# Kernel tuning notes

Hardware: AMD Instinct MI355X
Metric: run time of the kernel (lower is better)

The kernel has to match this reference:

```python
import jax, jax.numpy as jnp
import numpy as np

# constants matching init_kwargs
CLASSES = 80
CONF_T = 0.05
IOU_T = 0.5
MAX_DET = 100
MAX_DET_PER_CLASS = 100


def setup_inputs() -> dict:
    key = jax.random.key(0)
    k1, k2, k3, k4 = jax.random.split(key, 4)
    B, N = 8, 2048
    # structured predictions: [x1, y1, x2, y2, class, score] in a 640x640 image
    xy1 = jax.random.uniform(k1, (B, N, 2), dtype=jnp.float32) * 580.0
    wh = jax.random.uniform(k2, (B, N, 2), dtype=jnp.float32) * 60.0 + 1.0
    cls = jax.random.randint(k3, (B, N), 0, CLASSES).astype(jnp.float32)
    sc = jax.random.uniform(k4, (B, N), dtype=jnp.float32)
    predictions = jnp.concatenate([xy1, xy1 + wh, cls[..., None], sc[..., None]], axis=-1)
    return {"predictions": predictions}


def _pairwise_iou(b):
    # b: [B, N, 4] xyxy (IoU is invariant under xyxy<->yxyx swap used by the layer)
    x1, y1, x2, y2 = b[..., 0], b[..., 1], b[..., 2], b[..., 3]
    area = jnp.maximum(x2 - x1, 0.0) * jnp.maximum(y2 - y1, 0.0)  # [B,N]
    ix1 = jnp.maximum(x1[:, :, None], x1[:, None, :])
    iy1 = jnp.maximum(y1[:, :, None], y1[:, None, :])
    ix2 = jnp.minimum(x2[:, :, None], x2[:, None, :])
    iy2 = jnp.minimum(y2[:, :, None], y2[:, None, :])
    inter = jnp.maximum(ix2 - ix1, 0.0) * jnp.maximum(iy2 - iy1, 0.0)  # [B,N,N]
    union = area[:, :, None] + area[:, None, :] - inter
    return inter / jnp.maximum(union, 1e-8)


def reference(predictions):
    # Combined per-class NMS. Because scores are one-hot over classes (score *
    # one_hot(class)), per-class NMS is equivalent to class-aware greedy NMS on
    # the globally score-sorted boxes where suppression only acts within a class.
    B, N, _ = predictions.shape
    boxes = predictions[..., :4]
    cls = predictions[..., 4].astype(jnp.int32)
    scores = predictions[..., 5]
    valid = scores > CONF_T

    # sort by score descending (invalid boxes pushed to the end)
    order = jnp.argsort(jnp.where(valid, scores, -jnp.inf), axis=1)[:, ::-1]  # [B,N]
    bsort = jnp.take_along_axis(boxes, order[..., None], axis=1)
    ssort = jnp.take_along_axis(scores, order, axis=1)
    csort = jnp.take_along_axis(cls, order, axis=1)
    vsort = jnp.take_along_axis(valid, order, axis=1)

    iou = _pairwise_iou(bsort)  # [B,N,N]
    same_cls = csort[:, :, None] == csort[:, None, :]
    sup_mat = same_cls & (iou > IOU_T)  # [B,N,N] bool

    idxs = jnp.arange(N)

    def body(i, keep):
        active = keep[:, i]  # [B] is box i still alive?
        sup = keep & sup_mat[:, i, :] & (idxs > i)[None, :]
        return jnp.where(active[:, None], keep & ~sup, keep)

    keep = jax.lax.fori_loop(0, N, body, vsort)  # [B,N]

    # per-class cap (max_detections_per_class): rank among kept boxes of same class
    oh = jax.nn.one_hot(csort, CLASSES, dtype=jnp.float32)  # [B,N,C]
    csum = jnp.cumsum(oh * keep[..., None].astype(jnp.float32), axis=1)
    rank = jnp.take_along_axis(csum, csort[..., None], axis=2)[..., 0]  # [B,N]
    keep = keep & (rank <= MAX_DET_PER_CLASS)

    # global top max_detections among kept boxes
    final = jnp.where(keep, ssort, -1.0)
    _, ti = jax.lax.top_k(final, MAX_DET)  # [B,MAX_DET]
    v = jnp.take_along_axis(keep, ti, axis=1)
    boxes_out = jnp.where(v[..., None], jnp.take_along_axis(bsort, ti[..., None], axis=1), 0.0)
    scores_out = jnp.where(v, jnp.take_along_axis(ssort, ti, axis=1), 0.0)
    classes_out = jnp.where(v, jnp.take_along_axis(csort, ti, axis=1).astype(jnp.float32), 0.0)
    num_det = jnp.sum(v, axis=1).astype(jnp.int32)
    return boxes_out, scores_out, classes_out, num_det
```

## Files before the change

kernel.cpp:

```cpp
#include <hip/hip_runtime.h>
#include <stdint.h>

#define NB 2048
#define NCLASSES 80
#define CONF_T 0.05f
#define IOU_T 0.5f
#define MAX_DET 100
#define MAX_PER_CLASS 100

typedef unsigned long long u64;
typedef unsigned int u32;
typedef unsigned char u8;

__device__ __forceinline__ u64 shfl_xor_u64(u64 v, int mask) {
    int lo = (int)(u32)v, hi = (int)(u32)(v >> 32);
    lo = __shfl_xor(lo, mask, 64);
    hi = __shfl_xor(hi, mask, 64);
    return ((u64)(u32)hi << 32) | (u32)lo;
}

__device__ __forceinline__ int sbucket(u32 bits) {
    int b = (int)(bits >> 17) - 0x1E80;
    return b < 0 ? 0 : (b > 511 ? 511 : b);
}

__global__ __launch_bounds__(512) void k_class(const float* __restrict__ pred,
                                               u8* __restrict__ supBytes) {
    const int idx = blockIdx.x, tid = threadIdx.x;
    const int lane = tid & 63, wave = tid >> 6;

    __shared__ __align__(16) char smem[49152];
    float2* csS  = (float2*)smem;
    u64*    wkey = (u64*)(smem + 16384);
    float4* wb4  = (float4*)(smem + 20480);
    u64*    wm   = (u64*)(smem + 28672);
    u8*     fst  = (u8*)(smem + 32768);

    const int b = idx / 10;
    const int c = (idx % 10) * 8 + wave;
    const float* P = pred + (size_t)b * NB * 6;
    u8* sb = supBytes + (size_t)b * NB;

    for (int i = tid; i < NB; i += 512)
        csS[i] = *reinterpret_cast<const float2*>(P + i * 6 + 4);
    __syncthreads();

    u64* wkeyW = wkey + wave * 64;
    float4* wb4W = wb4 + wave * 64;
    u64* wmW = wm + wave * 64;

    int cnt = 0;
    for (int base = 0; base < NB; base += 64) {
        int i = base + lane;
        float2 cs = csS[i];
        bool v = (cs.y > CONF_T) && ((int)cs.x == c);
        u64 m = __ballot(v);
        if (v) {
            int pos = cnt + __popcll(m & ((1ull << lane) - 1ull));
            if (pos < 64) {
                float2 p01 = *reinterpret_cast<const float2*>(P + i * 6);
                float2 p23 = *reinterpret_cast<const float2*>(P + i * 6 + 2);
                wkeyW[pos] = ((u64)__float_as_uint(cs.y) << 32) | (u32)i;
                wb4W[pos] = make_float4(p01.x, p01.y, p23.x, p23.y);
            }
        }
        cnt += __popcll(m);
    }
    __builtin_amdgcn_wave_barrier();

    if (cnt <= 64) {
        u64 mykey = 0ull; int orig = 0;
        float x1 = 0.f, y1 = 0.f, x2 = 0.f, y2 = 0.f, ar = 0.f;
        if (lane < cnt) {
            mykey = wkeyW[lane];
            orig = (int)(u32)mykey;
            float4 bx = wb4W[lane];
            x1 = bx.x; y1 = bx.y; x2 = bx.z; y2 = bx.w;
            ar = fmaxf(x2 - x1, 0.f) * fmaxf(y2 - y1, 0.f);
        }
        u64 mj = 0ull;
        if (lane < cnt) {
            for (int i = 0; i < cnt; ++i) {
                u64 ki = wkeyW[i];
                if (ki > mykey) {
                    float4 bi = wb4W[i];
                    float ari = fmaxf(bi.z - bi.x, 0.f) * fmaxf(bi.w - bi.y, 0.f);
                    float ix1 = fmaxf(bi.x, x1), iy1 = fmaxf(bi.y, y1);
                    float ix2 = fminf(bi.z, x2), iy2 = fminf(bi.w, y2);
                    float inter = fmaxf(ix2 - ix1, 0.f) * fmaxf(iy2 - iy1, 0.f);
                    float uni = ari + ar - inter;
                    if (inter / fmaxf(uni, 1e-8f) > IOU_T) mj |= 1ull << i;
                }
            }
        }
        u64 conf = __ballot(mj != 0ull);
        bool sup = false;
        if (conf != 0ull) {
            u64 srcs = mj;
            #pragma unroll
            for (int d = 1; d < 64; d <<= 1) srcs |= shfl_xor_u64(srcs, d);
            wmW[lane] = mj;
            __builtin_amdgcn_wave_barrier();
            u64 Cset = srcs | conf;
            u64 keptS2 = 0ull, rem = Cset;
            while (rem) {
                u64 t = rem, bestk = 0ull; int bi = -1;
                while (t) {
                    int i = __ffsll(t) - 1; t &= t - 1;
                    u64 k = wkeyW[i];
                    if (k > bestk) { bestk = k; bi = i; }
                }
                rem &= ~(1ull << bi);
                if ((wmW[bi] & keptS2) == 0ull) keptS2 |= 1ull << bi;
            }
            sup = (mj & keptS2) != 0ull;
        }
        if (lane < cnt) sb[orig] = sup ? 1 : 0;
    } else {
        volatile u8* vf = fst + wave * NB;
        for (int o = lane; o < NB; o += 64) vf[o] = 0;
        __builtin_amdgcn_wave_barrier();
        int keptCount = 0;
        for (;;) {
            u64 best = 0ull; int bo = -1;
            for (int o = lane; o < NB; o += 64) {
                if (vf[o]) continue;
                float2 cs = csS[o];
                if (cs.y > CONF_T && (int)cs.x == c) {
                    u64 k = ((u64)__float_as_uint(cs.y) << 32) | (u32)o;
                    if (k > best) { best = k; bo = o; }
                }
            }
            for (int d = 32; d >= 1; d >>= 1) {
                u64 ob = shfl_xor_u64(best, d);
                int obo = __shfl_xor(bo, d, 64);
                if (ob > best) { best = ob; bo = obo; }
            }
            if (best == 0ull) break;
            keptCount++;
            int orig = (int)(u32)best;
            if (lane == 0) {
                vf[orig] = 1;
                sb[orig] = (keptCount > MAX_PER_CLASS) ? 1 : 0;
            }
            __builtin_amdgcn_wave_barrier();
            const float* q = P + orig * 6;
            float ax1 = q[0], ay1 = q[1], ax2 = q[2], ay2 = q[3];
            float aar = fmaxf(ax2 - ax1, 0.f) * fmaxf(ay2 - ay1, 0.f);
            for (int o = lane; o < NB; o += 64) {
                if (vf[o]) continue;
                float2 cs = csS[o];
                if (cs.y > CONF_T && (int)cs.x == c) {
                    const float* q2 = P + o * 6;
                    float bx1 = q2[0], by1 = q2[1], bx2 = q2[2], by2 = q2[3];
                    float br = fmaxf(bx2 - bx1, 0.f) * fmaxf(by2 - by1, 0.f);
                    float ix1 = fmaxf(ax1, bx1), iy1 = fmaxf(ay1, by1);
                    float ix2 = fminf(ax2, bx2), iy2 = fminf(ay2, by2);
                    float inter = fmaxf(ix2 - ix1, 0.f) * fmaxf(iy2 - iy1, 0.f);
                    if (inter / fmaxf(aar + br - inter, 1e-8f) > IOU_T) {
                        vf[o] = 2;
                        sb[o] = 1;
                    }
                }
            }
            __builtin_amdgcn_wave_barrier();
        }
    }
}

__global__ __launch_bounds__(256) void k_sel(const float* __restrict__ pred,
                                             const u8* __restrict__ supBytes,
                                             float* __restrict__ out, int B) {
    const int b = blockIdx.x, tid = threadIdx.x;
    __shared__ u32 smw[NB / 4];
    __shared__ int hist[512];
    __shared__ u64 cand[256];
    __shared__ u64 skey[NB];
    __shared__ int candCnt, TS, keptT;

    const float* P = pred + (size_t)b * NB * 6;
    const u32* sw = (const u32*)(supBytes + (size_t)b * NB);
    for (int i = tid; i < NB / 4; i += 256) smw[i] = sw[i];
    for (int i = tid; i < 512; i += 256) hist[i] = 0;
    if (tid == 0) candCnt = 0;
    __syncthreads();

    u64 kreg[8];
    #pragma unroll
    for (int t = 0; t < 8; ++t) {
        int i = tid + t * 256;
        float s = P[i * 6 + 5];
        bool sup = ((smw[i >> 2] >> ((i & 3) * 8)) & 0xFFu) != 0u;
        u64 kk = 0ull;
        if (s > CONF_T && !sup) {
            u32 bits = __float_as_uint(s);
            kk = ((u64)bits << 32) | (u32)i;
            atomicAdd(&hist[sbucket(bits)], 1);
        }
        kreg[t] = kk;
    }
    __syncthreads();

    if (tid < 64) {
        int h[8], s = 0;
        #pragma unroll
        for (int t = 0; t < 8; ++t) { h[t] = hist[tid * 8 + t]; s += h[t]; }
        int v = s;
        #pragma unroll
        for (int d = 1; d < 64; d <<= 1) {
            int t2 = __shfl_down(v, d, 64);
            if (tid + d < 64) v += t2;
        }
        int total = __shfl(v, 0, 64);
        int target = total < MAX_DET ? total : MAX_DET;
        int run = v - s, bestB = -1;
        for (int t = 7; t >= 0; --t) {
            run += h[t];
            if (run >= target && bestB < 0) bestB = tid * 8 + t;
        }
        int T = bestB;
        #pragma unroll
        for (int d = 32; d >= 1; d >>= 1) {
            int o = __shfl_xor(T, d, 64);
            T = o > T ? o : T;
        }
        if (tid == 0) { TS = T; keptT = total; }
    }
    __syncthreads();

    const int T = TS;
    #pragma unroll
    for (int t = 0; t < 8; ++t) {
        u64 kk = kreg[t];
        if (kk != 0ull && sbucket((u32)(kk >> 32)) >= T) {
            int pos = atomicAdd(&candCnt, 1);
            if (pos < 256) cand[pos] = kk;
        }
    }
    __syncthreads();

    int cc = candCnt;
    if (cc <= 256) {
        if (tid < 64) {
            const int lane = tid;
            const int iA = lane, iB = 64 + lane, iC = 128 + lane, iD = 192 + lane;
            u64 A  = (iA < cc) ? cand[iA] : 0ull;
            u64 Bv = (iB < cc) ? cand[iB] : 0ull;
            u64 C  = (iC < cc) ? cand[iC] : 0ull;
            u64 D  = (iD < cc) ? cand[iD] : 0ull;

            auto loc = [&](u64& X, u64& Y, int ix, int k) {
                bool up = ((ix & k) == 0);
                u64 mx = X > Y ? X : Y, mn = X > Y ? Y : X;
                X = up ? mx : mn; Y = up ? mn : mx;
            };
            auto shf = [&](u64& V, int iv, int j, int k) {
                u64 p = shfl_xor_u64(V, j);
                bool low = ((lane & j) == 0);
                bool up  = ((iv & k) == 0);
                V = (low == up) ? (V > p ? V : p) : (V < p ? V : p);
            };
            for (int k = 2; k <= 256; k <<= 1) {
                int jstart = k >> 1;
                if (jstart >= 128) { loc(A, C, iA, k); loc(Bv, D, iB, k); }
                if (jstart >= 64)  { loc(A, Bv, iA, k); loc(C, D, iC, k); }
                for (int j = (jstart > 32 ? 32 : jstart); j >= 1; j >>= 1) {
                    shf(A, iA, j, k); shf(Bv, iB, j, k); shf(C, iC, j, k); shf(D, iD, j, k);
                }
            }
            skey[iA] = A; skey[iB] = Bv; skey[iC] = C; skey[iD] = D;
        }
    } else {
        #pragma unroll
        for (int t = 0; t < 8; ++t) skey[tid + t * 256] = kreg[t];
        __syncthreads();
        for (int k = 2; k <= NB; k <<= 1)
            for (int j = k >> 1; j > 0; j >>= 1) {
                for (int pp = tid; pp < (NB >> 1); pp += 256) {
                    int i1 = ((pp & ~(j - 1)) << 1) | (pp & (j - 1));
                    int i2 = i1 + j;
                    bool up = ((i1 & k) == 0);
                    u64 a = skey[i1], c2 = skey[i2];
                    if (up ? (a < c2) : (a > c2)) { skey[i1] = c2; skey[i2] = a; }
                }
                __syncthreads();
            }
    }
    __syncthreads();

    float* boxes_out   = out + (size_t)b * MAX_DET * 4;
    float* scores_out  = out + (size_t)B * MAX_DET * 4 + (size_t)b * MAX_DET;
    float* classes_out = out + (size_t)B * MAX_DET * 5 + (size_t)b * MAX_DET;
    float* numdet_out  = out + (size_t)B * MAX_DET * 6 + b;

    int nd = keptT < MAX_DET ? keptT : MAX_DET;
    if (tid < MAX_DET) {
        if (tid < nd) {
            u64 kk = skey[tid];
            int orig = (int)(u32)kk;
            const float* q = P + orig * 6;
            boxes_out[tid * 4 + 0] = q[0];
            boxes_out[tid * 4 + 1] = q[1];
            boxes_out[tid * 4 + 2] = q[2];
            boxes_out[tid * 4 + 3] = q[3];
            scores_out[tid]  = __uint_as_float((u32)(kk >> 32));
            classes_out[tid] = q[4];
        } else {
            boxes_out[tid * 4 + 0] = 0.f;
            boxes_out[tid * 4 + 1] = 0.f;
            boxes_out[tid * 4 + 2] = 0.f;
            boxes_out[tid * 4 + 3] = 0.f;
            scores_out[tid]  = 0.f;
            classes_out[tid] = 0.f;
        }
    }
    if (tid == 0) *numdet_out = (float)nd;
}

__global__ __launch_bounds__(1024) void nms_fallback(const float* __restrict__ pred,
                                                     float* __restrict__ out, int B) {
    const int b = blockIdx.x, tid = threadIdx.x;
    __shared__ u64 keys[NB];
    __shared__ float bx1[NB], by1[NB], bx2[NB], by2[NB];
    __shared__ int kc[NB];
    __shared__ int cnt[NCLASSES];
    __shared__ int overflow;
    const float* P = pred + (size_t)b * NB * 6;
    for (int i = tid; i < NB; i += 1024) {
        float s = P[i * 6 + 5];
        keys[i] = (s > CONF_T) ? (((u64)__float_as_uint(s) << 32) | (uint32_t)i)
                               : (u64)(uint32_t)i;
    }
    __syncthreads();
    for (int k = 2; k <= NB; k <<= 1)
        for (int j = k >> 1; j > 0; j >>= 1) {
            for (int i = tid; i < NB; i += 1024) {
                int ixj = i ^ j;
                if (ixj > i) {
                    u64 a = keys[i], c = keys[ixj];
                    bool up = ((i & k) == 0);
                    if (up ? (a < c) : (a > c)) { keys[i] = c; keys[ixj] = a; }
                }
            }
            __syncthreads();
        }
    for (int i = tid; i < NB; i += 1024) {
        u64 k = keys[i];
        int orig = (int)(uint32_t)k;
        const float* q = P + orig * 6;
        bx1[i] = q[0]; by1[i] = q[1]; bx2[i] = q[2]; by2[i] = q[3];
        kc[i] = ((k >> 32) != 0) ? (int)q[4] : -1;
    }
    __syncthreads();
    bool dirty = false;
    for (int i = 0; i < NB - 1; ++i) {
        if (i == 0 || dirty) { __syncthreads(); dirty = false; }
        int ci = kc[i];
        if (ci < 0) continue;
        dirty = true;
        float x1i = bx1[i], y1i = by1[i], x2i = bx2[i], y2i = by2[i];
        float ai = fmaxf(x2i - x1i, 0.f) * fmaxf(y2i - y1i, 0.f);
        for (int j = i + 1 + tid; j < NB; j += 1024) {
            if (kc[j] != ci) continue;
            float ix1 = fmaxf(x1i, bx1[j]), iy1 = fmaxf(y1i, by1[j]);
            float ix2 = fminf(x2i, bx2[j]), iy2 = fminf(y2i, by2[j]);
            float inter = fmaxf(ix2 - ix1, 0.f) * fmaxf(iy2 - iy1, 0.f);
            float aj = fmaxf(bx2[j] - bx1[j], 0.f) * fmaxf(by2[j] - by1[j], 0.f);
            if (inter / fmaxf(ai + aj - inter, 1e-8f) > IOU_T) kc[j] = -1;
        }
    }
    __syncthreads();
    for (int i = tid; i < NCLASSES; i += 1024) cnt[i] = 0;
    if (tid == 0) overflow = 0;
    __syncthreads();
    for (int i = tid; i < NB; i += 1024) if (kc[i] >= 0) atomicAdd(&cnt[kc[i]], 1);
    __syncthreads();
    if (tid < NCLASSES && cnt[tid] > MAX_PER_CLASS) atomicOr(&overflow, 1);
    __syncthreads();
    if (overflow) {
        if (tid == 0) {
            for (int c = 0; c < NCLASSES; ++c) cnt[c] = 0;
            for (int i = 0; i < NB; ++i)
                if (kc[i] >= 0 && ++cnt[kc[i]] > MAX_PER_CLASS) kc[i] = -1;
        }
        __syncthreads();
    }
    if (tid < 64) {
        const int lane = tid;
        float* boxes_out   = out + (size_t)b * MAX_DET * 4;
        float* scores_out  = out + (size_t)B * MAX_DET * 4 + (size_t)b * MAX_DET;
        float* classes_out = out + (size_t)B * MAX_DET * 5 + (size_t)b * MAX_DET;
        float* numdet_out  = out + (size_t)B * MAX_DET * 6 + b;
        int running = 0;
        for (int chunk = 0; chunk < NB / 64; ++chunk) {
            int j = chunk * 64 + lane;
            int c = kc[j];
            bool k = (c >= 0);
            u64 m = __ballot(k);
            int pos = running + __popcll(m & ((1ull << lane) - 1ull));
            if (k && pos < MAX_DET) {
                boxes_out[pos * 4 + 0] = bx1[j];
                boxes_out[pos * 4 + 1] = by1[j];
                boxes_out[pos * 4 + 2] = bx2[j];
                boxes_out[pos * 4 + 3] = by2[j];
                scores_out[pos]  = __uint_as_float((uint32_t)(keys[j] >> 32));
                classes_out[pos] = (float)c;
            }
            running += __popcll(m);
        }
        int nd = running < MAX_DET ? running : MAX_DET;
        for (int p = nd + lane; p < MAX_DET; p += 64) {
            boxes_out[p * 4 + 0] = 0.f; boxes_out[p * 4 + 1] = 0.f;
            boxes_out[p * 4 + 2] = 0.f; boxes_out[p * 4 + 3] = 0.f;
            scores_out[p] = 0.f; classes_out[p] = 0.f;
        }
        if (lane == 0) *numdet_out = (float)nd;
    }
}

extern "C" void kernel_launch(void* const* d_in, const int* in_sizes, int n_in,
                              void* d_out, int out_size, void* d_ws, size_t ws_size,
                              hipStream_t stream) {
    const float* pred = (const float*)d_in[0];
    float* out = (float*)d_out;
    const int B = in_sizes[0] / (NB * 6);

    u8* supBytes = (u8*)d_ws;
    const size_t need = (size_t)B * NB;

    if (B != 8 || ws_size < need) {
        nms_fallback<<<B, 1024, 0, stream>>>(pred, out, B);
        return;
    }

    k_class<<<B * 10, 512, 0, stream>>>(pred, supBytes);
    k_sel<<<B, 256, 0, stream>>>(pred, supBytes, out, B);
}
```

Measured before the change: 29.82 us.

## Fuse per-class NMS and selection kernels via atomic completion counters

Merges the per-class suppression kernel and the per-batch selection kernel into one launch. The extra blocks at the end of the grid spin-wait on a per-batch done counter that the class blocks increment after a threadfence. This aims to remove the second kernel launch gap. In exchange it adds a hipMemsetAsync on the counters and relies on all class blocks being scheduled alongside the spinning selector blocks, which could deadlock if they are not co-resident.

```diff
diff --git a/kernel.cpp b/kernel.cpp
--- a/kernel.cpp
+++ b/kernel.cpp
@@ -24,297 +24,311 @@
     return b < 0 ? 0 : (b > 511 ? 511 : b);
 }
 
-__global__ __launch_bounds__(512) void k_class(const float* __restrict__ pred,
-                                               u8* __restrict__ supBytes) {
-    const int idx = blockIdx.x, tid = threadIdx.x;
+__global__ __launch_bounds__(512) void nms_single(const float* __restrict__ pred,
+                                                  u8* __restrict__ supBytes,
+                                                  u32* __restrict__ done,
+                                                  float* __restrict__ out, int B) {
+    const int bid = blockIdx.x, tid = threadIdx.x;
     const int lane = tid & 63, wave = tid >> 6;
 
     __shared__ __align__(16) char smem[49152];
-    float2* csS  = (float2*)smem;
-    u64*    wkey = (u64*)(smem + 16384);
-    float4* wb4  = (float4*)(smem + 20480);
-    u64*    wm   = (u64*)(smem + 28672);
-    u8*     fst  = (u8*)(smem + 32768);
-
-    const int b = idx / 10;
-    const int c = (idx % 10) * 8 + wave;
-    const float* P = pred + (size_t)b * NB * 6;
-    u8* sb = supBytes + (size_t)b * NB;
-
-    for (int i = tid; i < NB; i += 512)
-        csS[i] = *reinterpret_cast<const float2*>(P + i * 6 + 4);
-    __syncthreads();
-
-    u64* wkeyW = wkey + wave * 64;
-    float4* wb4W = wb4 + wave * 64;
-    u64* wmW = wm + wave * 64;
-
-    int cnt = 0;
-    for (int base = 0; base < NB; base += 64) {
-        int i = base + lane;
-        float2 cs = csS[i];
-        bool v = (cs.y > CONF_T) && ((int)cs.x == c);
-        u64 m = __ballot(v);
-        if (v) {
-            int pos = cnt + __popcll(m & ((1ull << lane) - 1ull));
-            if (pos < 64) {
-                float2 p01 = *reinterpret_cast<const float2*>(P + i * 6);
-                float2 p23 = *reinterpret_cast<const float2*>(P + i * 6 + 2);
-                wkeyW[pos] = ((u64)__float_as_uint(cs.y) << 32) | (u32)i;
-                wb4W[pos] = make_float4(p01.x, p01.y, p23.x, p23.y);
-            }
-        }
-        cnt += __popcll(m);
-    }
-    __builtin_amdgcn_wave_barrier();
-
-    if (cnt <= 64) {
-        u64 mykey = 0ull; int orig = 0;
-        float x1 = 0.f, y1 = 0.f, x2 = 0.f, y2 = 0.f, ar = 0.f;
-        if (lane < cnt) {
-            mykey = wkeyW[lane];
-            orig = (int)(u32)mykey;
-            float4 bx = wb4W[lane];
-            x1 = bx.x; y1 = bx.y; x2 = bx.z; y2 = bx.w;
-            ar = fmaxf(x2 - x1, 0.f) * fmaxf(y2 - y1, 0.f);
-        }
-        u64 mj = 0ull;
-        if (lane < cnt) {
-            for (int i = 0; i < cnt; ++i) {
-                u64 ki = wkeyW[i];
-                if (ki > mykey) {
-                    float4 bi = wb4W[i];
-                    float ari = fmaxf(bi.z - bi.x, 0.f) * fmaxf(bi.w - bi.y, 0.f);
-                    float ix1 = fmaxf(bi.x, x1), iy1 = fmaxf(bi.y, y1);
-                    float ix2 = fminf(bi.z, x2), iy2 = fminf(bi.w, y2);
-                    float inter = fmaxf(ix2 - ix1, 0.f) * fmaxf(iy2 - iy1, 0.f);
-                    float uni = ari + ar - inter;
-                    if (inter / fmaxf(uni, 1e-8f) > IOU_T) mj |= 1ull << i;
-                }
-            }
-        }
-        u64 conf = __ballot(mj != 0ull);
-        bool sup = false;
-        if (conf != 0ull) {
-            u64 srcs = mj;
+
+    if (bid < B * 10) {
+        float2* csS  = (float2*)smem;
+        u64*    wkey = (u64*)(smem + 16384);
+        float4* wb4  = (float4*)(smem + 20480);
+        u64*    wm   = (u64*)(smem + 28672);
+        u8*     fst  = (u8*)(smem + 32768);
+
+        const int b = bid / 10;
+        const int c = (bid % 10) * 8 + wave;
+        const float* P = pred + (size_t)b * NB * 6;
+        u8* sb = supBytes + (size_t)b * NB;
+
+        for (int i = tid; i < NB; i += 512)
+            csS[i] = *reinterpret_cast<const float2*>(P + i * 6 + 4);
+        __syncthreads();
+
+        u64* wkeyW = wkey + wave * 64;
+        float4* wb4W = wb4 + wave * 64;
+        u64* wmW = wm + wave * 64;
+
+        int cnt = 0;
+        for (int base = 0; base < NB; base += 64) {
+            int i = base + lane;
+            float2 cs = csS[i];
+            bool v = (cs.y > CONF_T) && ((int)cs.x == c);
+            u64 m = __ballot(v);
+            if (v) {
+                int pos = cnt + __popcll(m & ((1ull << lane) - 1ull));
+                if (pos < 64) {
+                    float2 p01 = *reinterpret_cast<const float2*>(P + i * 6);
+                    float2 p23 = *reinterpret_cast<const float2*>(P + i * 6 + 2);
+                    wkeyW[pos] = ((u64)__float_as_uint(cs.y) << 32) | (u32)i;
+                    wb4W[pos] = make_float4(p01.x, p01.y, p23.x, p23.y);
+                }
+            }
+            cnt += __popcll(m);
+        }
+        __builtin_amdgcn_wave_barrier();
+
+        if (cnt <= 64) {
+            u64 mykey = 0ull; int orig = 0;
+            float x1 = 0.f, y1 = 0.f, x2 = 0.f, y2 = 0.f, ar = 0.f;
+            if (lane < cnt) {
+                mykey = wkeyW[lane];
+                orig = (int)(u32)mykey;
+                float4 bx = wb4W[lane];
+                x1 = bx.x; y1 = bx.y; x2 = bx.z; y2 = bx.w;
+                ar = fmaxf(x2 - x1, 0.f) * fmaxf(y2 - y1, 0.f);
+            }
+            u64 mj = 0ull;
+            if (lane < cnt) {
+                for (int i = 0; i < cnt; ++i) {
+                    u64 ki = wkeyW[i];
+                    if (ki > mykey) {
+                        float4 bi = wb4W[i];
+                        float ari = fmaxf(bi.z - bi.x, 0.f) * fmaxf(bi.w - bi.y, 0.f);
+                        float ix1 = fmaxf(bi.x, x1), iy1 = fmaxf(bi.y, y1);
+                        float ix2 = fminf(bi.z, x2), iy2 = fminf(bi.w, y2);
+                        float inter = fmaxf(ix2 - ix1, 0.f) * fmaxf(iy2 - iy1, 0.f);
+                        float uni = ari + ar - inter;
+                        if (inter / fmaxf(uni, 1e-8f) > IOU_T) mj |= 1ull << i;
+                    }
+                }
+            }
+            u64 conf = __ballot(mj != 0ull);
+            bool sup = false;
+            if (conf != 0ull) {
+                u64 srcs = mj;
+                #pragma unroll
+                for (int d = 1; d < 64; d <<= 1) srcs |= shfl_xor_u64(srcs, d);
+                wmW[lane] = mj;
+                __builtin_amdgcn_wave_barrier();
+                u64 Cset = srcs | conf;
+                u64 keptS2 = 0ull, rem = Cset;
+                while (rem) {
+                    u64 t = rem, bestk = 0ull; int bi = -1;
+                    while (t) {
+                        int i = __ffsll(t) - 1; t &= t - 1;
+                        u64 k = wkeyW[i];
+                        if (k > bestk) { bestk = k; bi = i; }
+                    }
+                    rem &= ~(1ull << bi);
+                    if ((wmW[bi] & keptS2) == 0ull) keptS2 |= 1ull << bi;
+                }
+                sup = (mj & keptS2) != 0ull;
+            }
+            if (lane < cnt) sb[orig] = sup ? 1 : 0;
+        } else {
+            volatile u8* vf = fst + wave * NB;
+            for (int o = lane; o < NB; o += 64) vf[o] = 0;
+            __builtin_amdgcn_wave_barrier();
+            int keptCount = 0;
+            for (;;) {
+                u64 best = 0ull; int bo = -1;
+                for (int o = lane; o < NB; o += 64) {
+                    if (vf[o]) continue;
+                    float2 cs = csS[o];
+                    if (cs.y > CONF_T && (int)cs.x == c) {
+                        u64 k = ((u64)__float_as_uint(cs.y) << 32) | (u32)o;
+                        if (k > best) { best = k; bo = o; }
+                    }
+                }
+                for (int d = 32; d >= 1; d >>= 1) {
+                    u64 ob = shfl_xor_u64(best, d);
+                    int obo = __shfl_xor(bo, d, 64);
+                    if (ob > best) { best = ob; bo = obo; }
+                }
+                if (best == 0ull) break;
+                keptCount++;
+                int orig = (int)(u32)best;
+                if (lane == 0) {
+                    vf[orig] = 1;
+                    sb[orig] = (keptCount > MAX_PER_CLASS) ? 1 : 0;
+                }
+                __builtin_amdgcn_wave_barrier();
+                const float* q = P + orig * 6;
+                float ax1 = q[0], ay1 = q[1], ax2 = q[2], ay2 = q[3];
+                float aar = fmaxf(ax2 - ax1, 0.f) * fmaxf(ay2 - ay1, 0.f);
+                for (int o = lane; o < NB; o += 64) {
+                    if (vf[o]) continue;
+                    float2 cs = csS[o];
+                    if (cs.y > CONF_T && (int)cs.x == c) {
+                        const float* q2 = P + o * 6;
+                        float bx1 = q2[0], by1 = q2[1], bx2 = q2[2], by2 = q2[3];
+                        float br = fmaxf(bx2 - bx1, 0.f) * fmaxf(by2 - by1, 0.f);
+                        float ix1 = fmaxf(ax1, bx1), iy1 = fmaxf(ay1, by1);
+                        float ix2 = fminf(ax2, bx2), iy2 = fminf(ay2, by2);
+                        float inter = fmaxf(ix2 - ix1, 0.f) * fmaxf(iy2 - iy1, 0.f);
+                        if (inter / fmaxf(aar + br - inter, 1e-8f) > IOU_T) {
+                            vf[o] = 2;
+                            sb[o] = 1;
+                        }
+                    }
+                }
+                __builtin_amdgcn_wave_barrier();
+            }
+        }
+
+        __syncthreads();
+        if (tid == 0) { __threadfence(); atomicAdd(&done[b], 1u); }
+    } else {
+        u32* smw  = (u32*)smem;
+        int* hist = (int*)(smem + 2048);
+        u64* cand = (u64*)(smem + 4096);
+        u64* skey = (u64*)(smem + 8192);
+        __shared__ int candCnt, TS, keptT;
+
+        const int b = bid - B * 10;
+        const float* P = pred + (size_t)b * NB * 6;
+
+        for (int i = tid; i < 512; i += 512) hist[i] = 0;
+        if (tid == 0) candCnt = 0;
+
+        if (tid == 0)
+            while (atomicAdd(&done[b], 0u) < 10u)
+                __builtin_amdgcn_s_sleep(8);
+        __syncthreads();
+        __threadfence();
+        {
+            u32* sw = (u32*)(supBytes + (size_t)b * NB);
+            for (int i = tid; i < NB / 4; i += 512)
+                smw[i] = atomicOr(sw + i, 0u);
+        }
+        __syncthreads();
+
+        u64 kreg[4];
+        #pragma unroll
+        for (int t = 0; t < 4; ++t) {
+            int i = tid + t * 512;
+            float s = P[i * 6 + 5];
+            bool sup = ((smw[i >> 2] >> ((i & 3) * 8)) & 0xFFu) != 0u;
+            u64 kk = 0ull;
+            if (s > CONF_T && !sup) {
+                u32 bits = __float_as_uint(s);
+                kk = ((u64)bits << 32) | (u32)i;
+                atomicAdd(&hist[sbucket(bits)], 1);
+            }
+            kreg[t] = kk;
+        }
+        __syncthreads();
+
+        if (tid < 64) {
+            int h[8], s = 0;
             #pragma unroll
-            for (int d = 1; d < 64; d <<= 1) srcs |= shfl_xor_u64(srcs, d);
-            wmW[lane] = mj;
-            __builtin_amdgcn_wave_barrier();
-            u64 Cset = srcs | conf;
-            u64 keptS2 = 0ull, rem = Cset;
-            while (rem) {
-                u64 t = rem, bestk = 0ull; int bi = -1;
-                while (t) {
-                    int i = __ffsll(t) - 1; t &= t - 1;
-                    u64 k = wkeyW[i];
-                    if (k > bestk) { bestk = k; bi = i; }
-                }
-                rem &= ~(1ull << bi);
-                if ((wmW[bi] & keptS2) == 0ull) keptS2 |= 1ull << bi;
-            }
-            sup = (mj & keptS2) != 0ull;
-        }
-        if (lane < cnt) sb[orig] = sup ? 1 : 0;
-    } else {
-        volatile u8* vf = fst + wave * NB;
-        for (int o = lane; o < NB; o += 64) vf[o] = 0;
-        __builtin_amdgcn_wave_barrier();
-        int keptCount = 0;
-        for (;;) {
-            u64 best = 0ull; int bo = -1;
-            for (int o = lane; o < NB; o += 64) {
-                if (vf[o]) continue;
-                float2 cs = csS[o];
-                if (cs.y > CONF_T && (int)cs.x == c) {
-                    u64 k = ((u64)__float_as_uint(cs.y) << 32) | (u32)o;
-                    if (k > best) { best = k; bo = o; }
-                }
-            }
+            for (int t = 0; t < 8; ++t) { h[t] = hist[tid * 8 + t]; s += h[t]; }
+            int v = s;
+            #pragma unroll
+            for (int d = 1; d < 64; d <<= 1) {
+                int t2 = __shfl_down(v, d, 64);
+                if (tid + d < 64) v += t2;
+            }
+            int total = __shfl(v, 0, 64);
+            int target = total < MAX_DET ? total : MAX_DET;
+            int run = v - s, bestB = -1;
+            for (int t = 7; t >= 0; --t) {
+                run += h[t];
+                if (run >= target && bestB < 0) bestB = tid * 8 + t;
+            }
+            int T = bestB;
+            #pragma unroll
             for (int d = 32; d >= 1; d >>= 1) {
-                u64 ob = shfl_xor_u64(best, d);
-                int obo = __shfl_xor(bo, d, 64);
-                if (ob > best) { best = ob; bo = obo; }
-            }
-            if (best == 0ull) break;
-            keptCount++;
-            int orig = (int)(u32)best;
-            if (lane == 0) {
-                vf[orig] = 1;
-                sb[orig] = (keptCount > MAX_PER_CLASS) ? 1 : 0;
-            }
-            __builtin_amdgcn_wave_barrier();
-            const float* q = P + orig * 6;
-            float ax1 = q[0], ay1 = q[1], ax2 = q[2], ay2 = q[3];
-            float aar = fmaxf(ax2 - ax1, 0.f) * fmaxf(ay2 - ay1, 0.f);
-            for (int o = lane; o < NB; o += 64) {
-                if (vf[o]) continue;
-                float2 cs = csS[o];
-                if (cs.y > CONF_T && (int)cs.x == c) {
-                    const float* q2 = P + o * 6;
-                    float bx1 = q2[0], by1 = q2[1], bx2 = q2[2], by2 = q2[3];
-                    float br = fmaxf(bx2 - bx1, 0.f) * fmaxf(by2 - by1, 0.f);
-                    float ix1 = fmaxf(ax1, bx1), iy1 = fmaxf(ay1, by1);
-                    float ix2 = fminf(ax2, bx2), iy2 = fminf(ay2, by2);
-                    float inter = fmaxf(ix2 - ix1, 0.f) * fmaxf(iy2 - iy1, 0.f);
-                    if (inter / fmaxf(aar + br - inter, 1e-8f) > IOU_T) {
-                        vf[o] = 2;
-                        sb[o] = 1;
-                    }
-                }
-            }
-            __builtin_amdgcn_wave_barrier();
-        }
-    }
-}
-
-__global__ __launch_bounds__(256) void k_sel(const float* __restrict__ pred,
-                                             const u8* __restrict__ supBytes,
-                                             float* __restrict__ out, int B) {
-    const int b = blockIdx.x, tid = threadIdx.x;
-    __shared__ u32 smw[NB / 4];
-    __shared__ int hist[512];
-    __shared__ u64 cand[256];
-    __shared__ u64 skey[NB];
-    __shared__ int candCnt, TS, keptT;
-
-    const float* P = pred + (size_t)b * NB * 6;
-    const u32* sw = (const u32*)(supBytes + (size_t)b * NB);
-    for (int i = tid; i < NB / 4; i += 256) smw[i] = sw[i];
-    for (int i = tid; i < 512; i += 256) hist[i] = 0;
-    if (tid == 0) candCnt = 0;
-    __syncthreads();
-
-    u64 kreg[8];
-    #pragma unroll
-    for (int t = 0; t < 8; ++t) {
-        int i = tid + t * 256;
-        float s = P[i * 6 + 5];
-        bool sup = ((smw[i >> 2] >> ((i & 3) * 8)) & 0xFFu) != 0u;
-        u64 kk = 0ull;
-        if (s > CONF_T && !sup) {
-            u32 bits = __float_as_uint(s);
-            kk = ((u64)bits << 32) | (u32)i;
-            atomicAdd(&hist[sbucket(bits)], 1);
-        }
-        kreg[t] = kk;
-    }
-    __syncthreads();
-
-    if (tid < 64) {
-        int h[8], s = 0;
+                int o = __shfl_xor(T, d, 64);
+                T = o > T ? o : T;
+            }
+            if (tid == 0) { TS = T; keptT = total; }
+        }
+        __syncthreads();
+
+        const int T = TS;
         #pragma unroll
-        for (int t = 0; t < 8; ++t) { h[t] = hist[tid * 8 + t]; s += h[t]; }
-        int v = s;
-        #pragma unroll
-        for (int d = 1; d < 64; d <<= 1) {
-            int t2 = __shfl_down(v, d, 64);
-            if (tid + d < 64) v += t2;
-        }
-        int total = __shfl(v, 0, 64);
-        int target = total < MAX_DET ? total : MAX_DET;
-        int run = v - s, bestB = -1;
-        for (int t = 7; t >= 0; --t) {
-            run += h[t];
-            if (run >= target && bestB < 0) bestB = tid * 8 + t;
-        }
-        int T = bestB;
-        #pragma unroll
-        for (int d = 32; d >= 1; d >>= 1) {
-            int o = __shfl_xor(T, d, 64);
-            T = o > T ? o : T;
-        }
-        if (tid == 0) { TS = T; keptT = total; }
-    }
-    __syncthreads();
-
-    const int T = TS;
-    #pragma unroll
-    for (int t = 0; t < 8; ++t) {
-        u64 kk = kreg[t];
-        if (kk != 0ull && sbucket((u32)(kk >> 32)) >= T) {
-            int pos = atomicAdd(&candCnt, 1);
-            if (pos < 256) cand[pos] = kk;
-        }
-    }
-    __syncthreads();
-
-    int cc = candCnt;
-    if (cc <= 256) {
-        if (tid < 64) {
-            const int lane = tid;
-            const int iA = lane, iB = 64 + lane, iC = 128 + lane, iD = 192 + lane;
-            u64 A  = (iA < cc) ? cand[iA] : 0ull;
-            u64 Bv = (iB < cc) ? cand[iB] : 0ull;
-            u64 C  = (iC < cc) ? cand[iC] : 0ull;
-            u64 D  = (iD < cc) ? cand[iD] : 0ull;
-
-            auto loc = [&](u64& X, u64& Y, int ix, int k) {
-                bool up = ((ix & k) == 0);
-                u64 mx = X > Y ? X : Y, mn = X > Y ? Y : X;
-                X = up ? mx : mn; Y = up ? mn : mx;
-            };
-            auto shf = [&](u64& V, int iv, int j, int k) {
-                u64 p = shfl_xor_u64(V, j);
-                bool low = ((lane & j) == 0);
-                bool up  = ((iv & k) == 0);
-                V = (low == up) ? (V > p ? V : p) : (V < p ? V : p);
-            };
-            for (int k = 2; k <= 256; k <<= 1) {
-                int jstart = k >> 1;
-                if (jstart >= 128) { loc(A, C, iA, k); loc(Bv, D, iB, k); }
-                if (jstart >= 64)  { loc(A, Bv, iA, k); loc(C, D, iC, k); }
-                for (int j = (jstart > 32 ? 32 : jstart); j >= 1; j >>= 1) {
-                    shf(A, iA, j, k); shf(Bv, iB, j, k); shf(C, iC, j, k); shf(D, iD, j, k);
-                }
-            }
-            skey[iA] = A; skey[iB] = Bv; skey[iC] = C; skey[iD] = D;
-        }
-    } else {
-        #pragma unroll
-        for (int t = 0; t < 8; ++t) skey[tid + t * 256] = kreg[t];
-        __syncthreads();
-        for (int k = 2; k <= NB; k <<= 1)
-            for (int j = k >> 1; j > 0; j >>= 1) {
-                for (int pp = tid; pp < (NB >> 1); pp += 256) {
-                    int i1 = ((pp & ~(j - 1)) << 1) | (pp & (j - 1));
-                    int i2 = i1 + j;
-                    bool up = ((i1 & k) == 0);
-                    u64 a = skey[i1], c2 = skey[i2];
-                    if (up ? (a < c2) : (a > c2)) { skey[i1] = c2; skey[i2] = a; }
-                }
-                __syncthreads();
-            }
-    }
-    __syncthreads();
-
-    float* boxes_out   = out + (size_t)b * MAX_DET * 4;
-    float* scores_out  = out + (size_t)B * MAX_DET * 4 + (size_t)b * MAX_DET;
-    float* classes_out = out + (size_t)B * MAX_DET * 5 + (size_t)b * MAX_DET;
-    float* numdet_out  = out + (size_t)B * MAX_DET * 6 + b;
-
-    int nd = keptT < MAX_DET ? keptT : MAX_DET;
-    if (tid < MAX_DET) {
-        if (tid < nd) {
-            u64 kk = skey[tid];
-            int orig = (int)(u32)kk;
-            const float* q = P + orig * 6;
-            boxes_out[tid * 4 + 0] = q[0];
-            boxes_out[tid * 4 + 1] = q[1];
-            boxes_out[tid * 4 + 2] = q[2];
-            boxes_out[tid * 4 + 3] = q[3];
-            scores_out[tid]  = __uint_as_float((u32)(kk >> 32));
-            classes_out[tid] = q[4];
+        for (int t = 0; t < 4; ++t) {
+            u64 kk = kreg[t];
+            if (kk != 0ull && sbucket((u32)(kk >> 32)) >= T) {
+                int pos = atomicAdd(&candCnt, 1);
+                if (pos < 256) cand[pos] = kk;
+            }
+        }
+        __syncthreads();
+
+        int cc = candCnt;
+        if (cc <= 256) {
+            if (tid < 64) {
+                const int ln = tid;
+                const int iA = ln, iB = 64 + ln, iC = 128 + ln, iD = 192 + ln;
+                u64 A  = (iA < cc) ? cand[iA] : 0ull;
+                u64 Bv = (iB < cc) ? cand[iB] : 0ull;
+                u64 C  = (iC < cc) ? cand[iC] : 0ull;
+                u64 D  = (iD < cc) ? cand[iD] : 0ull;
+
+                auto loc = [&](u64& X, u64& Y, int ix, int k) {
+                    bool up = ((ix & k) == 0);
+                    u64 mx = X > Y ? X : Y, mn = X > Y ? Y : X;
+                    X = up ? mx : mn; Y = up ? mn : mx;
+                };
+                auto shf = [&](u64& V, int iv, int j, int k) {
+                    u64 p = shfl_xor_u64(V, j);
+                    bool low = ((ln & j) == 0);
+                    bool up  = ((iv & k) == 0);
+                    V = (low == up) ? (V > p ? V : p) : (V < p ? V : p);
+                };
+                for (int k = 2; k <= 256; k <<= 1) {
+                    int jstart = k >> 1;
+                    if (jstart >= 128) { loc(A, C, iA, k); loc(Bv, D, iB, k); }
+                    if (jstart >= 64)  { loc(A, Bv, iA, k); loc(C, D, iC, k); }
+                    for (int j = (jstart > 32 ? 32 : jstart); j >= 1; j >>= 1) {
+                        shf(A, iA, j, k); shf(Bv, iB, j, k); shf(C, iC, j, k); shf(D, iD, j, k);
+                    }
+                }
+                skey[iA] = A; skey[iB] = Bv; skey[iC] = C; skey[iD] = D;
+            }
         } else {
-            boxes_out[tid * 4 + 0] = 0.f;
-            boxes_out[tid * 4 + 1] = 0.f;
-            boxes_out[tid * 4 + 2] = 0.f;
-            boxes_out[tid * 4 + 3] = 0.f;
-            scores_out[tid]  = 0.f;
-            classes_out[tid] = 0.f;
-        }
-    }
-    if (tid == 0) *numdet_out = (float)nd;
+            #pragma unroll
+            for (int t = 0; t < 4; ++t) skey[tid + t * 512] = kreg[t];
+            __syncthreads();
+            for (int k = 2; k <= NB; k <<= 1)
+                for (int j = k >> 1; j > 0; j >>= 1) {
+                    for (int pp = tid; pp < (NB >> 1); pp += 512) {
+                        int i1 = ((pp & ~(j - 1)) << 1) | (pp & (j - 1));
+                        int i2 = i1 + j;
+                        bool up = ((i1 & k) == 0);
+                        u64 a = skey[i1], c2 = skey[i2];
+                        if (up ? (a < c2) : (a > c2)) { skey[i1] = c2; skey[i2] = a; }
+                    }
+                    __syncthreads();
+                }
+        }
+        __syncthreads();
+
+        float* boxes_out   = out + (size_t)b * MAX_DET * 4;
+        float* scores_out  = out + (size_t)B * MAX_DET * 4 + (size_t)b * MAX_DET;
+        float* classes_out = out + (size_t)B * MAX_DET * 5 + (size_t)b * MAX_DET;
+        float* numdet_out  = out + (size_t)B * MAX_DET * 6 + b;
+
+        int nd = keptT < MAX_DET ? keptT : MAX_DET;
+        if (tid < MAX_DET) {
+            if (tid < nd) {
+                u64 kk = skey[tid];
+                int orig = (int)(u32)kk;
+                const float* q = P + orig * 6;
+                boxes_out[tid * 4 + 0] = q[0];
+                boxes_out[tid * 4 + 1] = q[1];
+                boxes_out[tid * 4 + 2] = q[2];
+                boxes_out[tid * 4 + 3] = q[3];
+                scores_out[tid]  = __uint_as_float((u32)(kk >> 32));
+                classes_out[tid] = q[4];
+            } else {
+                boxes_out[tid * 4 + 0] = 0.f;
+                boxes_out[tid * 4 + 1] = 0.f;
+                boxes_out[tid * 4 + 2] = 0.f;
+                boxes_out[tid * 4 + 3] = 0.f;
+                scores_out[tid]  = 0.f;
+                classes_out[tid] = 0.f;
+            }
+        }
+        if (tid == 0) *numdet_out = (float)nd;
+    }
 }
 
 __global__ __launch_bounds__(1024) void nms_fallback(const float* __restrict__ pred,
@@ -426,13 +440,14 @@
     const int B = in_sizes[0] / (NB * 6);
 
     u8* supBytes = (u8*)d_ws;
-    const size_t need = (size_t)B * NB;
+    u32* done = (u32*)(supBytes + (size_t)B * NB);
+    const size_t need = (size_t)B * NB + (size_t)B * 4;
 
     if (B != 8 || ws_size < need) {
         nms_fallback<<<B, 1024, 0, stream>>>(pred, out, B);
         return;
     }
 
-    k_class<<<B * 10, 512, 0, stream>>>(pred, supBytes);
-    k_sel<<<B, 256, 0, stream>>>(pred, supBytes, out, B);
+    hipMemsetAsync(done, 0, (size_t)B * 4, stream);
+    nms_single<<<B * 10 + B, 512, 0, stream>>>(pred, supBytes, done, out, B);
 }
```

New measurement: 35.74 us. 1.2x slower.
